# Performance work log

Measured on AMD Instinct MI355X. Metric: run time of the kernel, lower is better.

## Reference

```python
import jax, jax.numpy as jnp
import numpy as np

B, N, XDIM, EDIM, H = 4, 256, 256, 128, 8
DF = XDIM // H


def _linear_params(key, din, dout):
    k1, k2 = jax.random.split(key)
    s = 1.0 / np.sqrt(din)
    W = jax.random.uniform(k1, (din, dout), minval=-s, maxval=s, dtype=jnp.float32)
    b = jax.random.uniform(k2, (dout,), minval=-s, maxval=s, dtype=jnp.float32)
    return W, b


def setup_inputs() -> dict:
    key = jax.random.key(0)
    ks = jax.random.split(key, 9)
    x = jax.random.normal(ks[0], (B, N, XDIM), dtype=jnp.float32)
    e = jax.random.normal(ks[1], (B, N, N, EDIM), dtype=jnp.float32)
    Wq, bq = _linear_params(ks[2], XDIM, XDIM)
    Wk, bk = _linear_params(ks[3], XDIM, XDIM)
    Wv, bv = _linear_params(ks[4], XDIM, XDIM)
    Wem, bem = _linear_params(ks[5], EDIM, XDIM)  # e_mul
    Wea, bea = _linear_params(ks[6], EDIM, XDIM)  # e_add
    Wxo, bxo = _linear_params(ks[7], XDIM, XDIM)  # x_out
    Weo, beo = _linear_params(ks[8], XDIM, EDIM)  # e_out
    return {"x": x, "e": e, "Wq": Wq, "bq": bq, "Wk": Wk, "bk": bk,
            "Wv": Wv, "bv": bv, "Wem": Wem, "bem": bem, "Wea": Wea, "bea": bea,
            "Wxo": Wxo, "bxo": bxo, "Weo": Weo, "beo": beo}


def reference(x, e, Wq, bq, Wk, bk, Wv, bv, Wem, bem, Wea, bea, Wxo, bxo, Weo, beo):
    Bq, Nq, _ = x.shape
    # per-node projections -> [B, N, H, DF]
    Q = (x @ Wq + bq).reshape(Bq, Nq, H, DF)
    K = (x @ Wk + bk).reshape(Bq, Nq, H, DF)
    V = (x @ Wv + bv).reshape(Bq, Nq, H, DF)
    # broadcasted outer product: Y[b,i,j,h,d] = Q[b,i,h,d] * K[b,j,h,d] / sqrt(DF)
    Y = Q[:, :, None] * K[:, None] * (1.0 / np.sqrt(DF))  # [B,N,N,H,DF]
    # edge modulation
    E1 = (e @ Wem + bem).reshape(Bq, Nq, Nq, H, DF)
    E2 = (e @ Wea + bea).reshape(Bq, Nq, Nq, H, DF)
    Y = Y * (E1 + 1.0) + E2
    # new edge features
    newE = Y.reshape(Bq, Nq, Nq, XDIM) @ Weo + beo  # [B,N,N,EDIM]
    # attention: softmax over the FIRST node axis (dim=1), as in the torch code
    attn = jax.nn.softmax(Y, axis=1)  # [B,N,N,H,DF]
    # weighted_V[b,j,h,d] = sum_i attn[b,i,j,h,d] * V[b,j,h,d]
    weighted_V = jnp.sum(attn * V[:, None], axis=1)  # [B,N,H,DF]
    newX = weighted_V.reshape(Bq, Nq, XDIM) @ Wxo + bxo  # [B,N,XDIM]
    return (newX, newE)
```

## Files before the change

kernel.cpp:

```cpp
#include <hip/hip_runtime.h>

#define NN 256
#define XD 256
#define ED 128

typedef __attribute__((ext_vector_type(8))) short short8;
typedef __attribute__((ext_vector_type(4))) float f32x4;

__device__ __forceinline__ unsigned short f2bf(float f) {
    unsigned u = __builtin_bit_cast(unsigned, f);
    u += 0x7FFF + ((u >> 16) & 1);
    return (unsigned short)(u >> 16);
}

#define MFMA16(a, b, c) __builtin_amdgcn_mfma_f32_16x16x32_bf16(a, b, c, 0, 0, 0)

__global__ __launch_bounds__(256) void wprep_kernel(
    const float* __restrict__ Wq, const float* __restrict__ Wk,
    const float* __restrict__ Wv, const float* __restrict__ Wxo,
    const float* __restrict__ Wem, const float* __restrict__ Wea,
    const float* __restrict__ Weo,
    short* __restrict__ WqT, short* __restrict__ WkT,
    short* __restrict__ WvT, short* __restrict__ WxoT,
    short* __restrict__ WemT, short* __restrict__ WeaT,
    short* __restrict__ WeoT)
{
    __shared__ float sT[32][33];
    int blk = blockIdx.x;
    const float* src; short* dst; int din, dout, tile;
    if (blk < 256) {
        int m = blk >> 6; tile = blk & 63; din = 256; dout = 256;
        src = m == 0 ? Wq : (m == 1 ? Wk : (m == 2 ? Wv : Wxo));
        dst = m == 0 ? WqT : (m == 1 ? WkT : (m == 2 ? WvT : WxoT));
    } else if (blk < 320) {
        int m = (blk - 256) >> 5; tile = (blk - 256) & 31; din = 128; dout = 256;
        src = m == 0 ? Wem : Wea; dst = m == 0 ? WemT : WeaT;
    } else {
        tile = blk - 320; din = 256; dout = 128;
        src = Weo; dst = WeoT;
    }
    int ksh = (din == 256) ? 3 : 2;
    int kt = tile & ((1 << ksh) - 1);
    int nt = tile >> ksh;
    int c = threadIdx.x & 31, rbase = threadIdx.x >> 5;
    #pragma unroll
    for (int p = 0; p < 4; ++p) {
        int r = rbase + p * 8;
        sT[r][c] = src[(kt * 32 + r) * dout + nt * 32 + c];
    }
    __syncthreads();
    #pragma unroll
    for (int p = 0; p < 4; ++p) {
        int r = rbase + p * 8;
        dst[(nt * 32 + r) * din + kt * 32 + c] = (short)f2bf(sT[c][r]);
    }
}

__global__ __launch_bounds__(512) void proj_qk_kernel(
    const float* __restrict__ x, const short* __restrict__ WqT,
    const short* __restrict__ WkT, const float* __restrict__ bq,
    const float* __restrict__ bk, float* __restrict__ Qs,
    float* __restrict__ KT)
{
    __shared__ unsigned short sX[64 * 264];
    const int blk = blockIdx.x;
    const int mtile = blk >> 1;
    const int mat   = blk & 1;
    const int tid = threadIdx.x, wave = tid >> 6, lane = tid & 63;
    const int quad = lane >> 4, l16 = lane & 15;

    {
        const float4* src4 = (const float4*)(x + (size_t)mtile * 64 * XD);
        #pragma unroll
        for (int it = 0; it < 8; ++it) {
            int idx4 = tid + it * 512;
            float4 v = src4[idx4];
            int elem = idx4 * 4, row = elem >> 8, col = elem & 255;
            short4 p = make_short4((short)f2bf(v.x), (short)f2bf(v.y),
                                   (short)f2bf(v.z), (short)f2bf(v.w));
            *(short4*)&sX[row * 264 + col] = p;
        }
    }
    __syncthreads();

    const short* WT   = mat ? WkT : WqT;
    const float* bias = mat ? bk : bq;
    const int c0 = wave * 32;

    f32x4 acc[4][2] = {};
    for (int ks = 0; ks < 8; ++ks) {
        short8 bfrag[2];
        #pragma unroll
        for (int ct = 0; ct < 2; ++ct)
            bfrag[ct] = *(const short8*)&WT[(c0 + ct * 16 + l16) * 256 + ks * 32 + quad * 8];
        #pragma unroll
        for (int mt = 0; mt < 4; ++mt) {
            short8 a = *(const short8*)&sX[(mt * 16 + l16) * 264 + ks * 32 + quad * 8];
            acc[mt][0] = MFMA16(a, bfrag[0], acc[mt][0]);
            acc[mt][1] = MFMA16(a, bfrag[1], acc[mt][1]);
        }
    }

    if (mat == 0) {
        #pragma unroll
        for (int mt = 0; mt < 4; ++mt)
            #pragma unroll
            for (int ct = 0; ct < 2; ++ct) {
                int cc = c0 + ct * 16 + l16;
                float bb = bias[cc];
                #pragma unroll
                for (int r = 0; r < 4; ++r)
                    Qs[(size_t)(mtile * 64 + mt * 16 + quad * 4 + r) * 256 + cc] =
                        (acc[mt][ct][r] + bb) * 0.17677669529663687f;
            }
    } else {
        int b = mtile >> 2, j0p = (mtile & 3) * 64;
        #pragma unroll
        for (int mt = 0; mt < 4; ++mt)
            #pragma unroll
            for (int ct = 0; ct < 2; ++ct) {
                int cc = c0 + ct * 16 + l16;
                float bb = bias[cc];
                f32x4 st;
                #pragma unroll
                for (int r = 0; r < 4; ++r) st[r] = acc[mt][ct][r] + bb;
                *(f32x4*)&KT[(size_t)(b * 256 + cc) * 256 + j0p + mt * 16 + quad * 4] = st;
            }
    }
}

__global__ __launch_bounds__(512) void proj_vx_kernel(
    const float* __restrict__ x, const short* __restrict__ WvT,
    const float* __restrict__ bv, const short* __restrict__ WxoT,
    const float* __restrict__ bxo, float* __restrict__ outX)
{
    __shared__ unsigned short sX[64 * 264];
    __shared__ unsigned short sV[64 * 264];
    const int mtile = blockIdx.x;
    const int tid = threadIdx.x, wave = tid >> 6, lane = tid & 63;
    const int quad = lane >> 4, l16 = lane & 15;

    {
        const float4* src4 = (const float4*)(x + (size_t)mtile * 64 * XD);
        #pragma unroll
        for (int it = 0; it < 8; ++it) {
            int idx4 = tid + it * 512;
            float4 v = src4[idx4];
            int elem = idx4 * 4, row = elem >> 8, col = elem & 255;
            short4 p = make_short4((short)f2bf(v.x), (short)f2bf(v.y),
                                   (short)f2bf(v.z), (short)f2bf(v.w));
            *(short4*)&sX[row * 264 + col] = p;
        }
    }
    __syncthreads();

    const int c0 = wave * 32;
    f32x4 acc[4][2] = {};
    for (int ks = 0; ks < 8; ++ks) {
        short8 bfrag[2];
        #pragma unroll
        for (int ct = 0; ct < 2; ++ct)
            bfrag[ct] = *(const short8*)&WvT[(c0 + ct * 16 + l16) * 256 + ks * 32 + quad * 8];
        #pragma unroll
        for (int mt = 0; mt < 4; ++mt) {
            short8 a = *(const short8*)&sX[(mt * 16 + l16) * 264 + ks * 32 + quad * 8];
            acc[mt][0] = MFMA16(a, bfrag[0], acc[mt][0]);
            acc[mt][1] = MFMA16(a, bfrag[1], acc[mt][1]);
        }
    }
    #pragma unroll
    for (int mt = 0; mt < 4; ++mt)
        #pragma unroll
        for (int ct = 0; ct < 2; ++ct) {
            int cc = c0 + ct * 16 + l16;
            float bb = bv[cc];
            #pragma unroll
            for (int r = 0; r < 4; ++r)
                sV[(mt * 16 + quad * 4 + r) * 264 + cc] = f2bf(acc[mt][ct][r] + bb);
        }
    __syncthreads();

    f32x4 acc2[4][2] = {};
    for (int ks = 0; ks < 8; ++ks) {
        short8 bfrag[2];
        #pragma unroll
        for (int ct = 0; ct < 2; ++ct)
            bfrag[ct] = *(const short8*)&WxoT[(c0 + ct * 16 + l16) * 256 + ks * 32 + quad * 8];
        #pragma unroll
        for (int mt = 0; mt < 4; ++mt) {
            short8 a = *(const short8*)&sV[(mt * 16 + l16) * 264 + ks * 32 + quad * 8];
            acc2[mt][0] = MFMA16(a, bfrag[0], acc2[mt][0]);
            acc2[mt][1] = MFMA16(a, bfrag[1], acc2[mt][1]);
        }
    }
    #pragma unroll
    for (int mt = 0; mt < 4; ++mt)
        #pragma unroll
        for (int ct = 0; ct < 2; ++ct) {
            int cc = c0 + ct * 16 + l16;
            float bb = bxo[cc];
            #pragma unroll
            for (int r = 0; r < 4; ++r)
                outX[(size_t)(mtile * 64 + mt * 16 + quad * 4 + r) * 256 + cc] =
                    acc2[mt][ct][r] + bb;
        }
}

__global__ __launch_bounds__(256, 3) void fused_edge_kernel(
    const float* __restrict__ e, const float* __restrict__ Qs,
    const float* __restrict__ KT, const short* __restrict__ WemT,
    const short* __restrict__ WeaT, const short* __restrict__ WeoT,
    const float* __restrict__ bem, const float* __restrict__ bea,
    const float* __restrict__ beo, float* __restrict__ outE)
{
    __shared__ unsigned short sE[64 * 140];
    __shared__ unsigned short sY[64 * 268];

    const int blk  = blockIdx.x;
    const int jq   = blk & 3;
    const int i    = (blk >> 2) & 255;
    const int b    = blk >> 10;
    const int j0   = jq * 64;
    const int tid  = threadIdx.x;
    const int wave = tid >> 6;
    const int lane = tid & 63;
    const int quad = lane >> 4;
    const int l16  = lane & 15;

    {
        const float4* src4 = (const float4*)(e + (size_t)((b * NN + i) * NN + j0) * ED);
        #pragma unroll
        for (int it = 0; it < 8; ++it) {
            int idx4 = tid + it * 256;
            float4 v = src4[idx4];
            int elem = idx4 * 4, row = elem >> 7, col = elem & 127;
            short4 p = make_short4((short)f2bf(v.x), (short)f2bf(v.y),
                                   (short)f2bf(v.z), (short)f2bf(v.w));
            *(short4*)&sE[row * 140 + col] = p;
        }
    }

    const float* Qrow = Qs + (size_t)(b * NN + i) * XD;
    float bo[2];
    #pragma unroll
    for (int ct = 0; ct < 2; ++ct) bo[ct] = beo[wave * 32 + ct * 16 + l16];

    __syncthreads();

    #pragma unroll
    for (int p = 0; p < 2; ++p) {
        const int c0 = wave * 32 + p * 128;
        float qsv[2], bmv[2], bav[2];
        int ktA[2];
        #pragma unroll
        for (int ct = 0; ct < 2; ++ct) {
            int cc = c0 + ct * 16 + l16;
            qsv[ct] = Qrow[cc];
            bmv[ct] = bem[cc] + 1.0f;
            bav[ct] = bea[cc];
            ktA[ct] = (b * 256 + cc) * 256 + j0 + quad * 4;
        }
        short8 B1[4][2], B2[4][2];
        #pragma unroll
        for (int ks = 0; ks < 4; ++ks)
            #pragma unroll
            for (int ct = 0; ct < 2; ++ct) {
                int n = c0 + ct * 16 + l16;
                B1[ks][ct] = *(const short8*)&WemT[n * 128 + ks * 32 + quad * 8];
                B2[ks][ct] = *(const short8*)&WeaT[n * 128 + ks * 32 + quad * 8];
            }
        #pragma unroll
        for (int mc = 0; mc < 4; ++mc) {
            const int m0 = mc * 16;
            f32x4 aE1[2] = {}, aE2[2] = {};
            __builtin_amdgcn_s_setprio(1);
            #pragma unroll
            for (int ks = 0; ks < 4; ++ks) {
                short8 a = *(const short8*)&sE[(m0 + l16) * 140 + ks * 32 + quad * 8];
                aE1[0] = MFMA16(a, B1[ks][0], aE1[0]);
                aE1[1] = MFMA16(a, B1[ks][1], aE1[1]);
                aE2[0] = MFMA16(a, B2[ks][0], aE2[0]);
                aE2[1] = MFMA16(a, B2[ks][1], aE2[1]);
            }
            __builtin_amdgcn_s_setprio(0);
            #pragma unroll
            for (int ct = 0; ct < 2; ++ct) {
                f32x4 kv = *(const f32x4*)&KT[ktA[ct] + m0];
                int cc = c0 + ct * 16 + l16;
                #pragma unroll
                for (int r = 0; r < 4; ++r) {
                    float y = qsv[ct] * kv[r] * (aE1[ct][r] + bmv[ct])
                              + (aE2[ct][r] + bav[ct]);
                    sY[(m0 + quad * 4 + r) * 268 + cc] = f2bf(y);
                }
            }
        }
    }
    __syncthreads();

    short8 B3[8][2];
    #pragma unroll
    for (int ks = 0; ks < 8; ++ks)
        #pragma unroll
        for (int ct = 0; ct < 2; ++ct)
            B3[ks][ct] = *(const short8*)&WeoT[(wave * 32 + ct * 16 + l16) * 256 + ks * 32 + quad * 8];
    f32x4 acc2[4][2] = {};
    __builtin_amdgcn_s_setprio(1);
    #pragma unroll
    for (int ks = 0; ks < 8; ++ks) {
        #pragma unroll
        for (int mt = 0; mt < 4; ++mt) {
            short8 a = *(const short8*)&sY[(mt * 16 + l16) * 268 + ks * 32 + quad * 8];
            acc2[mt][0] = MFMA16(a, B3[ks][0], acc2[mt][0]);
            acc2[mt][1] = MFMA16(a, B3[ks][1], acc2[mt][1]);
        }
    }
    __builtin_amdgcn_s_setprio(0);
    float* outBase = outE + (size_t)((b * NN + i) * NN + j0) * ED;
    #pragma unroll
    for (int mt = 0; mt < 4; ++mt)
        #pragma unroll
        for (int ct = 0; ct < 2; ++ct) {
            int col = wave * 32 + ct * 16 + l16;
            #pragma unroll
            for (int r = 0; r < 4; ++r)
                outBase[(size_t)(mt * 16 + quad * 4 + r) * ED + col] = acc2[mt][ct][r] + bo[ct];
        }
}

extern "C" void kernel_launch(void* const* d_in, const int* in_sizes, int n_in,
                              void* d_out, int out_size, void* d_ws, size_t ws_size,
                              hipStream_t stream)
{
    const float* x   = (const float*)d_in[0];
    const float* e   = (const float*)d_in[1];
    const float* Wq  = (const float*)d_in[2];
    const float* bq  = (const float*)d_in[3];
    const float* Wk  = (const float*)d_in[4];
    const float* bk  = (const float*)d_in[5];
    const float* Wv  = (const float*)d_in[6];
    const float* bv  = (const float*)d_in[7];
    const float* Wem = (const float*)d_in[8];
    const float* bem = (const float*)d_in[9];
    const float* Wea = (const float*)d_in[10];
    const float* bea = (const float*)d_in[11];
    const float* Wxo = (const float*)d_in[12];
    const float* bxo = (const float*)d_in[13];
    const float* Weo = (const float*)d_in[14];
    const float* beo = (const float*)d_in[15];

    float* outX = (float*)d_out;
    float* outE = (float*)d_out + 262144;

    float* Qs   = (float*)d_ws;
    float* KT   = Qs + 262144;
    short* WqT  = (short*)(KT + 262144);
    short* WkT  = WqT + 65536;
    short* WvT  = WkT + 65536;
    short* WxoT = WvT + 65536;
    short* WemT = WxoT + 65536;
    short* WeaT = WemT + 32768;
    short* WeoT = WeaT + 32768;

    hipLaunchKernelGGL(wprep_kernel, dim3(352), dim3(256), 0, stream,
                       Wq, Wk, Wv, Wxo, Wem, Wea, Weo,
                       WqT, WkT, WvT, WxoT, WemT, WeaT, WeoT);
    hipLaunchKernelGGL(proj_qk_kernel, dim3(32), dim3(512), 0, stream,
                       x, WqT, WkT, bq, bk, Qs, KT);
    hipLaunchKernelGGL(proj_vx_kernel, dim3(16), dim3(512), 0, stream,
                       x, WvT, bv, WxoT, bxo, outX);
    hipLaunchKernelGGL(fused_edge_kernel, dim3(4096), dim3(256), 0, stream,
                       e, Qs, KT, WemT, WeaT, WeoT, bem, bea, beo, outE);
}
```

Before: 366.0 us.

## Double fused edge kernel block to 512 threads, halving per-wave tile work

The fused edge kernel now runs 8 waves per block instead of 4. Each wave covers half as many output columns in both the E1/E2 projection stage and the Weo output GEMM, which cuts per-thread register arrays (B fragments, accumulators) roughly in half. Launch bounds target 6 blocks of 512 per CU to raise occupancy and latency hiding. The tradeoff is more redundant loads of shared A fragments from LDS per MFMA, and LDS capacity may cap how many blocks are actually resident.

```diff
diff --git a/kernel.cpp b/kernel.cpp
--- a/kernel.cpp
+++ b/kernel.cpp
@@ -206,7 +206,7 @@
         }
 }
 
-__global__ __launch_bounds__(256, 3) void fused_edge_kernel(
+__global__ __launch_bounds__(512, 6) void fused_edge_kernel(
     const float* __restrict__ e, const float* __restrict__ Qs,
     const float* __restrict__ KT, const short* __restrict__ WemT,
     const short* __restrict__ WeaT, const short* __restrict__ WeoT,
@@ -230,8 +230,8 @@
     {
         const float4* src4 = (const float4*)(e + (size_t)((b * NN + i) * NN + j0) * ED);
         #pragma unroll
-        for (int it = 0; it < 8; ++it) {
-            int idx4 = tid + it * 256;
+        for (int it = 0; it < 4; ++it) {
+            int idx4 = tid + it * 512;
             float4 v = src4[idx4];
             int elem = idx4 * 4, row = elem >> 7, col = elem & 127;
             short4 p = make_short4((short)f2bf(v.x), (short)f2bf(v.y),
@@ -241,78 +241,60 @@
     }
 
     const float* Qrow = Qs + (size_t)(b * NN + i) * XD;
-    float bo[2];
-    #pragma unroll
-    for (int ct = 0; ct < 2; ++ct) bo[ct] = beo[wave * 32 + ct * 16 + l16];
-
-    __syncthreads();
-
-    #pragma unroll
-    for (int p = 0; p < 2; ++p) {
-        const int c0 = wave * 32 + p * 128;
-        float qsv[2], bmv[2], bav[2];
-        int ktA[2];
-        #pragma unroll
-        for (int ct = 0; ct < 2; ++ct) {
-            int cc = c0 + ct * 16 + l16;
-            qsv[ct] = Qrow[cc];
-            bmv[ct] = bem[cc] + 1.0f;
-            bav[ct] = bea[cc];
-            ktA[ct] = (b * 256 + cc) * 256 + j0 + quad * 4;
-        }
-        short8 B1[4][2], B2[4][2];
-        #pragma unroll
-        for (int ks = 0; ks < 4; ++ks)
-            #pragma unroll
-            for (int ct = 0; ct < 2; ++ct) {
-                int n = c0 + ct * 16 + l16;
-                B1[ks][ct] = *(const short8*)&WemT[n * 128 + ks * 32 + quad * 8];
-                B2[ks][ct] = *(const short8*)&WeaT[n * 128 + ks * 32 + quad * 8];
-            }
+    const float bo = beo[wave * 16 + l16];
+
+    __syncthreads();
+
+    #pragma unroll
+    for (int ct = 0; ct < 2; ++ct) {
+        const int c0 = wave * 32 + ct * 16;
+        const int cc = c0 + l16;
+        const float qsv = Qrow[cc];
+        const float bmv = bem[cc] + 1.0f;
+        const float bav = bea[cc];
+        const int   ktA = (b * 256 + cc) * 256 + j0 + quad * 4;
+
+        short8 B1[4], B2[4];
+        #pragma unroll
+        for (int ks = 0; ks < 4; ++ks) {
+            B1[ks] = *(const short8*)&WemT[cc * 128 + ks * 32 + quad * 8];
+            B2[ks] = *(const short8*)&WeaT[cc * 128 + ks * 32 + quad * 8];
+        }
         #pragma unroll
         for (int mc = 0; mc < 4; ++mc) {
             const int m0 = mc * 16;
-            f32x4 aE1[2] = {}, aE2[2] = {};
+            f32x4 kv = *(const f32x4*)&KT[ktA + m0];
+            f32x4 aE1 = {}, aE2 = {};
             __builtin_amdgcn_s_setprio(1);
             #pragma unroll
             for (int ks = 0; ks < 4; ++ks) {
                 short8 a = *(const short8*)&sE[(m0 + l16) * 140 + ks * 32 + quad * 8];
-                aE1[0] = MFMA16(a, B1[ks][0], aE1[0]);
-                aE1[1] = MFMA16(a, B1[ks][1], aE1[1]);
-                aE2[0] = MFMA16(a, B2[ks][0], aE2[0]);
-                aE2[1] = MFMA16(a, B2[ks][1], aE2[1]);
+                aE1 = MFMA16(a, B1[ks], aE1);
+                aE2 = MFMA16(a, B2[ks], aE2);
             }
             __builtin_amdgcn_s_setprio(0);
             #pragma unroll
-            for (int ct = 0; ct < 2; ++ct) {
-                f32x4 kv = *(const f32x4*)&KT[ktA[ct] + m0];
-                int cc = c0 + ct * 16 + l16;
-                #pragma unroll
-                for (int r = 0; r < 4; ++r) {
-                    float y = qsv[ct] * kv[r] * (aE1[ct][r] + bmv[ct])
-                              + (aE2[ct][r] + bav[ct]);
-                    sY[(m0 + quad * 4 + r) * 268 + cc] = f2bf(y);
-                }
+            for (int r = 0; r < 4; ++r) {
+                float y = qsv * kv[r] * (aE1[r] + bmv) + (aE2[r] + bav);
+                sY[(m0 + quad * 4 + r) * 268 + cc] = f2bf(y);
             }
         }
     }
     __syncthreads();
 
-    short8 B3[8][2];
+    const int ow = wave * 16;
+    short8 B3[8];
     #pragma unroll
     for (int ks = 0; ks < 8; ++ks)
-        #pragma unroll
-        for (int ct = 0; ct < 2; ++ct)
-            B3[ks][ct] = *(const short8*)&WeoT[(wave * 32 + ct * 16 + l16) * 256 + ks * 32 + quad * 8];
-    f32x4 acc2[4][2] = {};
+        B3[ks] = *(const short8*)&WeoT[(ow + l16) * 256 + ks * 32 + quad * 8];
+    f32x4 acc2[4] = {};
     __builtin_amdgcn_s_setprio(1);
     #pragma unroll
     for (int ks = 0; ks < 8; ++ks) {
         #pragma unroll
         for (int mt = 0; mt < 4; ++mt) {
             short8 a = *(const short8*)&sY[(mt * 16 + l16) * 268 + ks * 32 + quad * 8];
-            acc2[mt][0] = MFMA16(a, B3[ks][0], acc2[mt][0]);
-            acc2[mt][1] = MFMA16(a, B3[ks][1], acc2[mt][1]);
+            acc2[mt] = MFMA16(a, B3[ks], acc2[mt]);
         }
     }
     __builtin_amdgcn_s_setprio(0);
@@ -320,12 +302,8 @@
     #pragma unroll
     for (int mt = 0; mt < 4; ++mt)
         #pragma unroll
-        for (int ct = 0; ct < 2; ++ct) {
-            int col = wave * 32 + ct * 16 + l16;
-            #pragma unroll
-            for (int r = 0; r < 4; ++r)
-                outBase[(size_t)(mt * 16 + quad * 4 + r) * ED + col] = acc2[mt][ct][r] + bo[ct];
-        }
+        for (int r = 0; r < 4; ++r)
+            outBase[(size_t)(mt * 16 + quad * 4 + r) * ED + ow + l16] = acc2[mt][r] + bo;
 }
 
 extern "C" void kernel_launch(void* const* d_in, const int* in_sizes, int n_in,
@@ -369,6 +347,6 @@
                        x, WqT, WkT, bq, bk, Qs, KT);
     hipLaunchKernelGGL(proj_vx_kernel, dim3(16), dim3(512), 0, stream,
                        x, WvT, bv, WxoT, bxo, outX);
-    hipLaunchKernelGGL(fused_edge_kernel, dim3(4096), dim3(256), 0, stream,
+    hipLaunchKernelGGL(fused_edge_kernel, dim3(4096), dim3(512), 0, stream,
                        e, Qs, KT, WemT, WeaT, WeoT, bem, bea, beo, outE);
 }
```

Result: slower. 376.4 us (+2.9%).
